# Kernel tuning notes

Hardware: AMD Instinct MI355X
Metric: run time of the kernel (lower is better)

Reference implementation:

```python
import jax, jax.numpy as jnp
import numpy as np

N_NODES = 100000
N_EDGES = 640000
D_IN = 128
D_H = 128


def setup_inputs() -> dict:
    key = jax.random.key(0)
    ks = jax.random.split(key, 24)
    def W(k, shp):
        return jax.random.normal(k, shp, dtype=jnp.float32) * 0.05
    inp = {
        "x": jax.random.normal(ks[0], (N_NODES, D_IN), dtype=jnp.float32),
        "src": jax.random.randint(ks[1], (N_EDGES,), 0, N_NODES, dtype=jnp.int32),
        "dst": jax.random.randint(ks[2], (N_EDGES,), 0, N_NODES, dtype=jnp.int32),
        "neg_src": jax.random.randint(ks[3], (N_EDGES,), 0, N_NODES, dtype=jnp.int32),
        "neg_dst": jax.random.randint(ks[4], (N_EDGES,), 0, N_NODES, dtype=jnp.int32),
        # SAGEConv layer 1/2/3: fc_self weight, fc_neigh weight (stored [in,out]), bias
        "Ws1": W(ks[5], (D_IN, D_H)), "Wn1": W(ks[6], (D_IN, D_H)), "b1": jnp.zeros((D_H,), jnp.float32),
        "Ws2": W(ks[7], (D_H, D_H)), "Wn2": W(ks[8], (D_H, D_H)), "b2": jnp.zeros((D_H,), jnp.float32),
        "Ws3": W(ks[9], (D_H, D_H)), "Wn3": W(ks[10], (D_H, D_H)), "b3": jnp.zeros((D_H,), jnp.float32),
        # MLPPredictor: W1 [2h,h], W2 [h,1]
        "Wp1": W(ks[11], (2 * D_H, D_H)), "bp1": jnp.zeros((D_H,), jnp.float32),
        "Wp2": W(ks[12], (D_H, 1)), "bp2": jnp.zeros((1,), jnp.float32),
    }
    return inp


def _sage_mean(x, src, dst, Ws, Wn, b):
    # DGL SAGEConv 'mean': rst = fc_self(h) + fc_neigh(mean_{in-neighbors}(h)) + bias
    n = x.shape[0]
    msum = jax.ops.segment_sum(x[src], dst, num_segments=n)        # [N, d]
    deg = jax.ops.segment_sum(jnp.ones_like(src, dtype=x.dtype), dst, num_segments=n)
    mean = msum / jnp.clip(deg, 1.0)[:, None]                      # zero for isolated nodes
    return x @ Ws + mean @ Wn + b


def _edge_score(h, s, d, Wp1, bp1, Wp2, bp2):
    z = jnp.concatenate([h[s], h[d]], axis=1)                      # [E, 2h]
    return (jax.nn.relu(z @ Wp1 + bp1) @ Wp2 + bp2)[:, 0]          # [E]


def reference(x, src, dst, neg_src, neg_dst,
              Ws1, Wn1, b1, Ws2, Wn2, b2, Ws3, Wn3, b3,
              Wp1, bp1, Wp2, bp2):
    h = _sage_mean(x, src, dst, Ws1, Wn1, b1)
    h = _sage_mean(h, src, dst, Ws2, Wn2, b2)
    h = _sage_mean(h, src, dst, Ws3, Wn3, b3)
    pos = _edge_score(h, src, dst, Wp1, bp1, Wp2, bp2)
    neg = _edge_score(h, neg_src, neg_dst, Wp1, bp1, Wp2, bp2)
    return (pos, neg)
```

## Files before the change

kernel.cpp:

```cpp
#include <hip/hip_runtime.h>

#define N_NODES 100000
#define N_EDGES 640000
#define D 128
#define SCAN_TILE 1024
#define SCAN_BLOCKS ((N_NODES + SCAN_TILE - 1) / SCAN_TILE)

typedef __attribute__((ext_vector_type(8))) short bf16x8;
typedef __attribute__((ext_vector_type(4))) float f32x4;

__device__ __forceinline__ unsigned short f32_to_bf16(float f) {
  union { float f; unsigned int u; } v; v.f = f;
  unsigned int u = v.u;
  unsigned int r = (u + 0x7fffu + ((u >> 16) & 1u)) >> 16;
  return (unsigned short)r;
}
__device__ __forceinline__ float bf16_lo(unsigned int u) { return __uint_as_float(u << 16); }
__device__ __forceinline__ float bf16_hi(unsigned int u) { return __uint_as_float(u & 0xffff0000u); }

__device__ __forceinline__ void acc8(float* a, uint4 r) {
  a[0] += bf16_lo(r.x); a[1] += bf16_hi(r.x);
  a[2] += bf16_lo(r.y); a[3] += bf16_hi(r.y);
  a[4] += bf16_lo(r.z); a[5] += bf16_hi(r.z);
  a[6] += bf16_lo(r.w); a[7] += bf16_hi(r.w);
}

__global__ void zero_i32(int* __restrict__ p, int n) {
  int i = blockIdx.x * blockDim.x + threadIdx.x;
  if (i < n) p[i] = 0;
}

__global__ void f32_to_bf16_vec(const float* __restrict__ in, unsigned short* __restrict__ out, int n4) {
  int i = blockIdx.x * blockDim.x + threadIdx.x;
  if (i < n4) {
    float4 v = ((const float4*)in)[i];
    ushort4 o;
    o.x = f32_to_bf16(v.x); o.y = f32_to_bf16(v.y);
    o.z = f32_to_bf16(v.z); o.w = f32_to_bf16(v.w);
    ((ushort4*)out)[i] = o;
  }
}

__global__ void transpose_w(const float* __restrict__ W0, const float* __restrict__ W1,
                            const float* __restrict__ W2, const float* __restrict__ W3,
                            const float* __restrict__ W4, const float* __restrict__ W5,
                            const float* __restrict__ W6, const float* __restrict__ W7,
                            unsigned short* __restrict__ wt) {
  int id = blockIdx.x * 256 + threadIdx.x;
  int mat = id >> 14;
  int rem = id & 16383;
  int n = rem >> 7, k = rem & 127;
  const float* Wm = mat < 4 ? (mat < 2 ? (mat == 0 ? W0 : W1) : (mat == 2 ? W2 : W3))
                            : (mat < 6 ? (mat == 4 ? W4 : W5) : (mat == 6 ? W6 : W7));
  wt[id] = f32_to_bf16(Wm[k * D + n]);
}

__global__ void hist_kernel(const int* __restrict__ dst, int* __restrict__ deg, int E) {
  int i = blockIdx.x * blockDim.x + threadIdx.x;
  if (i < E) atomicAdd(&deg[dst[i]], 1);
}

__global__ void scan_blocksum(const int* __restrict__ deg, int* __restrict__ partial, int n) {
  __shared__ int lds[256];
  const int tid = threadIdx.x;
  const int base = blockIdx.x * SCAN_TILE + tid * 4;
  int s = 0;
#pragma unroll
  for (int j = 0; j < 4; ++j) {
    int i = base + j;
    if (i < n) s += deg[i];
  }
  lds[tid] = s;
  __syncthreads();
  for (int off = 128; off > 0; off >>= 1) {
    if (tid < off) lds[tid] += lds[tid + off];
    __syncthreads();
  }
  if (tid == 0) partial[blockIdx.x] = lds[0];
}

__global__ void scan_offsets(int* __restrict__ partial, int* __restrict__ row_start, int nb, int n) {
  __shared__ int lds[128];
  const int tid = threadIdx.x;
  int v = (tid < nb) ? partial[tid] : 0;
  lds[tid] = v;
  __syncthreads();
  for (int off = 1; off < 128; off <<= 1) {
    int t = (tid >= off) ? lds[tid - off] : 0;
    __syncthreads();
    lds[tid] += t;
    __syncthreads();
  }
  if (tid < nb) partial[tid] = (tid == 0) ? 0 : lds[tid - 1];
  if (tid == 0) row_start[n] = lds[nb - 1];
}

__global__ void scan_final(const int* __restrict__ deg, const int* __restrict__ partial,
                           int* __restrict__ row_start, int n) {
  __shared__ int lds[256];
  const int tid = threadIdx.x;
  const int base = blockIdx.x * SCAN_TILE + tid * 4;
  int d[4];
  int s = 0;
#pragma unroll
  for (int j = 0; j < 4; ++j) {
    int i = base + j;
    d[j] = (i < n) ? deg[i] : 0;
    s += d[j];
  }
  lds[tid] = s;
  __syncthreads();
  for (int off = 1; off < 256; off <<= 1) {
    int t = (tid >= off) ? lds[tid - off] : 0;
    __syncthreads();
    lds[tid] += t;
    __syncthreads();
  }
  int pre = partial[blockIdx.x] + lds[tid] - s;
#pragma unroll
  for (int j = 0; j < 4; ++j) {
    int i = base + j;
    if (i < n) {
      row_start[i] = pre;
      pre += d[j];
    }
  }
}

__global__ void fill_kernel(const int* __restrict__ src, const int* __restrict__ dst,
                            const int* __restrict__ row_start, int* __restrict__ cursor,
                            int* __restrict__ esrc, int E) {
  int i = blockIdx.x * blockDim.x + threadIdx.x;
  if (i < E) {
    int d = dst[i];
    int pos = atomicAdd(&cursor[d], 1);
    esrc[row_start[d] + pos] = src[i];
  }
}

__global__ __launch_bounds__(256) void gather_mean(
    const unsigned short* __restrict__ hin,
    const int* __restrict__ row_start, const int* __restrict__ esrc,
    unsigned short* __restrict__ mean, int M) {
  const int t = blockIdx.x * blockDim.x + threadIdx.x;
  const int node = t >> 4;
  const int fl = t & 15;
  if (node >= M) return;
  const int s0 = row_start[node], s1 = row_start[node + 1];
  float ac[8] = {0.f, 0.f, 0.f, 0.f, 0.f, 0.f, 0.f, 0.f};
  for (int e = s0; e < s1; e += 8) {
    int idx[8];
#pragma unroll
    for (int j = 0; j < 8; ++j) idx[j] = esrc[min(e + j, s1 - 1)];
    uint4 r[8];
#pragma unroll
    for (int j = 0; j < 8; ++j)
      r[j] = *(const uint4*)(hin + (((size_t)idx[j]) << 7) + fl * 8);
#pragma unroll
    for (int j = 0; j < 8; ++j)
      if (e + j < s1) acc8(ac, r[j]);
  }
  const float inv = 1.0f / (float)max(s1 - s0, 1);
#pragma unroll
  for (int k = 0; k < 8; ++k) ac[k] *= inv;
  uint4 o;
  o.x = (unsigned)f32_to_bf16(ac[0]) | ((unsigned)f32_to_bf16(ac[1]) << 16);
  o.y = (unsigned)f32_to_bf16(ac[2]) | ((unsigned)f32_to_bf16(ac[3]) << 16);
  o.z = (unsigned)f32_to_bf16(ac[4]) | ((unsigned)f32_to_bf16(ac[5]) << 16);
  o.w = (unsigned)f32_to_bf16(ac[6]) | ((unsigned)f32_to_bf16(ac[7]) << 16);
  *reinterpret_cast<uint4*>(mean + (((size_t)node) << 7) + fl * 8) = o;
}

template <bool PRED>
__global__ __launch_bounds__(256) void layer_mlp(
    const unsigned short* __restrict__ hin,
    const unsigned short* __restrict__ mean,
    const unsigned short* __restrict__ Wts, const unsigned short* __restrict__ Wtn,
    const float* __restrict__ bias,
    const unsigned short* __restrict__ WtA, const unsigned short* __restrict__ WtB,
    const float* __restrict__ biasA,
    unsigned short* __restrict__ out0, unsigned short* __restrict__ out1, int M) {
  __shared__ unsigned short wl[64][136];
  __shared__ unsigned short mt[PRED ? 64 : 1][136];
  const int tid = threadIdx.x;
  const int lane = tid & 63;
  const int wave = tid >> 6;
  const int m0 = blockIdx.x * 64;
  const int row = lane & 15;
  const int q = lane >> 4;
  const int mw = m0 + wave * 16;
  const int mload = min(mw + row, M - 1);
  const int lrow = wave * 16 + row;

  unsigned short (*et)[136];
  if constexpr (PRED) et = mt; else et = wl;

  auto stage64 = [&](const unsigned short* W, int half) {
#pragma unroll
    for (int i = 0; i < 4; ++i) {
      int seg = i * 256 + tid;
      int r = seg >> 4, o = (seg & 15) * 8;
      *reinterpret_cast<bf16x8*>(&wl[r][o]) =
          *reinterpret_cast<const bf16x8*>(W + (size_t)(half * 64 + r) * D + o);
    }
  };
  auto mfma_half = [&](bf16x8* a, f32x4* accp) {
#pragma unroll
    for (int s = 0; s < 4; ++s)
#pragma unroll
      for (int t = 0; t < 4; ++t) {
        bf16x8 b = *reinterpret_cast<const bf16x8*>(&wl[t * 16 + row][s * 32 + q * 8]);
        accp[t] = __builtin_amdgcn_mfma_f32_16x16x32_bf16(a[s], b, accp[t], 0, 0, 0);
      }
  };
  auto epilogue = [&](f32x4* accp, const float* bvec, unsigned short* dst, bool prebar) {
    if (prebar) __syncthreads();
#pragma unroll
    for (int t = 0; t < 8; ++t) {
      const int col = t * 16 + row;
      const float bv = bvec ? bvec[col] : 0.f;
#pragma unroll
      for (int r = 0; r < 4; ++r)
        et[wave * 16 + q * 4 + r][col] = f32_to_bf16(accp[t][r] + bv);
    }
    __syncthreads();
#pragma unroll
    for (int i = 0; i < 4; ++i) {
      int idx = i * 256 + tid;
      int r2 = idx >> 4;
      int c8 = (idx & 15) * 8;
      int m = m0 + r2;
      if (m < M)
        *reinterpret_cast<uint4*>(dst + (size_t)m * D + c8) =
            *reinterpret_cast<const uint4*>(&et[r2][c8]);
    }
  };

  stage64(Wts, 0);
  bf16x8 ah[4], am[4];
#pragma unroll
  for (int s = 0; s < 4; ++s) {
    ah[s] = *reinterpret_cast<const bf16x8*>(hin + (size_t)mload * D + s * 32 + q * 8);
    am[s] = *reinterpret_cast<const bf16x8*>(mean + (size_t)mload * D + s * 32 + q * 8);
  }
  __syncthreads();

  f32x4 acc[8];
#pragma unroll
  for (int t = 0; t < 8; ++t) acc[t] = (f32x4){0.f, 0.f, 0.f, 0.f};

  mfma_half(ah, acc);
  __syncthreads(); stage64(Wts, 1); __syncthreads();
  mfma_half(ah, acc + 4);
  __syncthreads(); stage64(Wtn, 0); __syncthreads();
  mfma_half(am, acc);
  __syncthreads(); stage64(Wtn, 1); __syncthreads();
  mfma_half(am, acc + 4);

  if (!PRED) {
    epilogue(acc, bias, out0, true);
    return;
  }

  __syncthreads();
#pragma unroll
  for (int t = 0; t < 8; ++t) {
    const int col = t * 16 + row;
    const float bv = bias[col];
#pragma unroll
    for (int r = 0; r < 4; ++r)
      mt[wave * 16 + q * 4 + r][col] = f32_to_bf16(acc[t][r] + bv);
  }
  stage64(WtA, 0);
  __syncthreads();
  bf16x8 ap[4];
#pragma unroll
  for (int s = 0; s < 4; ++s)
    ap[s] = *reinterpret_cast<const bf16x8*>(&mt[lrow][s * 32 + q * 8]);

#pragma unroll
  for (int t = 0; t < 8; ++t) acc[t] = (f32x4){0.f, 0.f, 0.f, 0.f};
  mfma_half(ap, acc);
  __syncthreads(); stage64(WtA, 1); __syncthreads();
  mfma_half(ap, acc + 4);
  epilogue(acc, biasA, out0, false);
  __syncthreads(); stage64(WtB, 0); __syncthreads();
#pragma unroll
  for (int t = 0; t < 8; ++t) acc[t] = (f32x4){0.f, 0.f, 0.f, 0.f};
  mfma_half(ap, acc);
  __syncthreads(); stage64(WtB, 1); __syncthreads();
  mfma_half(ap, acc + 4);
  epilogue(acc, nullptr, out1, false);
}

__device__ __forceinline__ float relu_dot8(uint4 a, uint4 b, float4 w0, float4 w1) {
  return fmaxf(bf16_lo(a.x) + bf16_lo(b.x), 0.f) * w0.x +
         fmaxf(bf16_hi(a.x) + bf16_hi(b.x), 0.f) * w0.y +
         fmaxf(bf16_lo(a.y) + bf16_lo(b.y), 0.f) * w0.z +
         fmaxf(bf16_hi(a.y) + bf16_hi(b.y), 0.f) * w0.w +
         fmaxf(bf16_lo(a.z) + bf16_lo(b.z), 0.f) * w1.x +
         fmaxf(bf16_hi(a.z) + bf16_hi(b.z), 0.f) * w1.y +
         fmaxf(bf16_lo(a.w) + bf16_lo(b.w), 0.f) * w1.z +
         fmaxf(bf16_hi(a.w) + bf16_hi(b.w), 0.f) * w1.w;
}

__global__ __launch_bounds__(256) void edge_score4(
    const unsigned short* __restrict__ A, const unsigned short* __restrict__ B,
    const int* __restrict__ ps, const int* __restrict__ pd,
    const int* __restrict__ ns, const int* __restrict__ nd,
    const float* __restrict__ Wp2, const float* __restrict__ bp2,
    float* __restrict__ out, int E) {
  const int t = blockIdx.x * blockDim.x + threadIdx.x;
  const int g2 = t >> 4;
  const int fl = t & 15;
  const int g = g2 >> 1;
  const int e0 = g * 4;
  if (e0 >= E) return;
  const bool neg = (g2 & 1) != 0;
  const int* ss = neg ? ns : ps;
  const int* dd = neg ? nd : pd;
  float* op = neg ? out + E : out;

  const int4 s4 = *(const int4*)(ss + e0);
  const int4 d4 = *(const int4*)(dd + e0);
  const float4 w0 = *(const float4*)(Wp2 + fl * 8);
  const float4 w1 = *(const float4*)(Wp2 + fl * 8 + 4);
  const size_t fo = (size_t)(fl * 8);

  uint4 a0 = *(const uint4*)(A + (((size_t)s4.x << 7) + fo));
  uint4 b0 = *(const uint4*)(B + (((size_t)d4.x << 7) + fo));
  uint4 a1 = *(const uint4*)(A + (((size_t)s4.y << 7) + fo));
  uint4 b1 = *(const uint4*)(B + (((size_t)d4.y << 7) + fo));
  uint4 a2 = *(const uint4*)(A + (((size_t)s4.z << 7) + fo));
  uint4 b2 = *(const uint4*)(B + (((size_t)d4.z << 7) + fo));
  uint4 a3 = *(const uint4*)(A + (((size_t)s4.w << 7) + fo));
  uint4 b3 = *(const uint4*)(B + (((size_t)d4.w << 7) + fo));

  float p0 = relu_dot8(a0, b0, w0, w1);
  float p1 = relu_dot8(a1, b1, w0, w1);
  float p2 = relu_dot8(a2, b2, w0, w1);
  float p3 = relu_dot8(a3, b3, w0, w1);

  p0 += __shfl_xor(p0, 1); p1 += __shfl_xor(p1, 1); p2 += __shfl_xor(p2, 1); p3 += __shfl_xor(p3, 1);
  p0 += __shfl_xor(p0, 2); p1 += __shfl_xor(p1, 2); p2 += __shfl_xor(p2, 2); p3 += __shfl_xor(p3, 2);
  p0 += __shfl_xor(p0, 4); p1 += __shfl_xor(p1, 4); p2 += __shfl_xor(p2, 4); p3 += __shfl_xor(p3, 4);
  p0 += __shfl_xor(p0, 8); p1 += __shfl_xor(p1, 8); p2 += __shfl_xor(p2, 8); p3 += __shfl_xor(p3, 8);

  if (fl == 0) {
    const float bv = bp2[0];
    *reinterpret_cast<float4*>(op + e0) = make_float4(p0 + bv, p1 + bv, p2 + bv, p3 + bv);
  }
}

extern "C" void kernel_launch(void* const* d_in, const int* in_sizes, int n_in,
                              void* d_out, int out_size, void* d_ws, size_t ws_size,
                              hipStream_t stream) {
  const float* x = (const float*)d_in[0];
  const int* src = (const int*)d_in[1];
  const int* dst = (const int*)d_in[2];
  const int* nsrc = (const int*)d_in[3];
  const int* ndst = (const int*)d_in[4];
  const float* Ws1 = (const float*)d_in[5];
  const float* Wn1 = (const float*)d_in[6];
  const float* b1 = (const float*)d_in[7];
  const float* Ws2 = (const float*)d_in[8];
  const float* Wn2 = (const float*)d_in[9];
  const float* b2 = (const float*)d_in[10];
  const float* Ws3 = (const float*)d_in[11];
  const float* Wn3 = (const float*)d_in[12];
  const float* b3 = (const float*)d_in[13];
  const float* Wp1 = (const float*)d_in[14];
  const float* bp1 = (const float*)d_in[15];
  const float* Wp2 = (const float*)d_in[16];
  const float* bp2 = (const float*)d_in[17];
  float* out = (float*)d_out;

  char* ws = (char*)d_ws;
  size_t off = 0;
  auto alloc = [&](size_t bytes) -> void* {
    void* p = ws + off;
    off += (bytes + 255) & ~(size_t)255;
    return p;
  };
  const size_t NODE_F32 = sizeof(float) * (size_t)N_NODES * D;
  char* region0 = (char*)alloc(NODE_F32);
  char* region1 = (char*)alloc(NODE_F32);
  unsigned short* meanb = (unsigned short*)alloc(sizeof(unsigned short) * (size_t)N_NODES * D);
  int* row_start = (int*)alloc(sizeof(int) * (N_NODES + 1));
  int* deg = (int*)alloc(sizeof(int) * N_NODES * 2);
  int* cursor = deg + N_NODES;
  int* esrc = (int*)alloc(sizeof(int) * N_EDGES);
  int* partial = (int*)alloc(sizeof(int) * 128);
  unsigned short* wt = (unsigned short*)alloc(sizeof(unsigned short) * 8 * D * D);
  (void)ws_size;

  unsigned short* xb = (unsigned short*)region0;
  unsigned short* hA = (unsigned short*)region1;
  unsigned short* hB = hA + (size_t)N_NODES * D;
  unsigned short* Ab = xb;
  unsigned short* Bb = xb + (size_t)N_NODES * D;

  f32_to_bf16_vec<<<(N_NODES * D / 4 + 255) / 256, 256, 0, stream>>>(x, xb, N_NODES * D / 4);
  transpose_w<<<512, 256, 0, stream>>>(Ws1, Wn1, Ws2, Wn2, Ws3, Wn3, Wp1, Wp1 + D * D, wt);

  zero_i32<<<(2 * N_NODES + 255) / 256, 256, 0, stream>>>(deg, 2 * N_NODES);
  hist_kernel<<<(N_EDGES + 255) / 256, 256, 0, stream>>>(dst, deg, N_EDGES);
  scan_blocksum<<<SCAN_BLOCKS, 256, 0, stream>>>(deg, partial, N_NODES);
  scan_offsets<<<1, 128, 0, stream>>>(partial, row_start, SCAN_BLOCKS, N_NODES);
  scan_final<<<SCAN_BLOCKS, 256, 0, stream>>>(deg, partial, row_start, N_NODES);
  fill_kernel<<<(N_EDGES + 255) / 256, 256, 0, stream>>>(src, dst, row_start, cursor, esrc, N_EDGES);

  const int gatherBlocks = (N_NODES * 16 + 255) / 256;
  const int mlpBlocks = (N_NODES + 63) / 64;
  const int edgeBlocks = (2 * (N_EDGES / 4) * 16) / 256;

  gather_mean<<<gatherBlocks, 256, 0, stream>>>(xb, row_start, esrc, meanb, N_NODES);
  layer_mlp<false><<<mlpBlocks, 256, 0, stream>>>(
      xb, meanb, wt, wt + 16384, b1, nullptr, nullptr, nullptr, hA, nullptr, N_NODES);
  gather_mean<<<gatherBlocks, 256, 0, stream>>>(hA, row_start, esrc, meanb, N_NODES);
  layer_mlp<false><<<mlpBlocks, 256, 0, stream>>>(
      hA, meanb, wt + 2 * 16384, wt + 3 * 16384, b2, nullptr, nullptr, nullptr, hB, nullptr, N_NODES);
  gather_mean<<<gatherBlocks, 256, 0, stream>>>(hB, row_start, esrc, meanb, N_NODES);
  layer_mlp<true><<<mlpBlocks, 256, 0, stream>>>(
      hB, meanb, wt + 4 * 16384, wt + 5 * 16384, b3, wt + 6 * 16384, wt + 7 * 16384, bp1,
      Ab, Bb, N_NODES);
  edge_score4<<<edgeBlocks, 256, 0, stream>>>(Ab, Bb, src, dst, nsrc, ndst, Wp2, bp2, out, N_EDGES);
}
```

Before: 450.6 us.

## Score edges via destination-sorted CSR to reuse destination row

Builds a combined CSR over the positive and negative edge sets, grouped by destination and recording original edge ids. The edge scoring kernel now runs one 16-lane group per destination node, loads the B row once and gathers only the A rows of its in-neighbours, then scatters scores back by edge id. This halves the random row gathers in scoring, but adds a second histogram, scan and fill pass, extra index arrays, scattered output writes and load imbalance from varying degrees.

```diff
diff --git a/kernel.cpp b/kernel.cpp
--- a/kernel.cpp
+++ b/kernel.cpp
@@ -4,7 +4,6 @@
 #define N_EDGES 640000
 #define D 128
 #define SCAN_TILE 1024
-#define SCAN_BLOCKS ((N_NODES + SCAN_TILE - 1) / SCAN_TILE)
 
 typedef __attribute__((ext_vector_type(8))) short bf16x8;
 typedef __attribute__((ext_vector_type(4))) float f32x4;
@@ -55,9 +54,13 @@
   wt[id] = f32_to_bf16(Wm[k * D + n]);
 }
 
-__global__ void hist_kernel(const int* __restrict__ dst, int* __restrict__ deg, int E) {
+__global__ void hist2_kernel(const int* __restrict__ dst, const int* __restrict__ ndst,
+                             int* __restrict__ deg2, int E) {
   int i = blockIdx.x * blockDim.x + threadIdx.x;
-  if (i < E) atomicAdd(&deg[dst[i]], 1);
+  if (i < E) {
+    atomicAdd(&deg2[dst[i]], 1);
+    atomicAdd(&deg2[N_NODES + ndst[i]], 1);
+  }
 }
 
 __global__ void scan_blocksum(const int* __restrict__ deg, int* __restrict__ partial, int n) {
@@ -79,13 +82,13 @@
   if (tid == 0) partial[blockIdx.x] = lds[0];
 }
 
-__global__ void scan_offsets(int* __restrict__ partial, int* __restrict__ row_start, int nb, int n) {
-  __shared__ int lds[128];
+__global__ void scan_offsets256(int* __restrict__ partial, int* __restrict__ row_start, int nb, int n) {
+  __shared__ int lds[256];
   const int tid = threadIdx.x;
   int v = (tid < nb) ? partial[tid] : 0;
   lds[tid] = v;
   __syncthreads();
-  for (int off = 1; off < 128; off <<= 1) {
+  for (int off = 1; off < 256; off <<= 1) {
     int t = (tid >= off) ? lds[tid - off] : 0;
     __syncthreads();
     lds[tid] += t;
@@ -127,14 +130,22 @@
   }
 }
 
-__global__ void fill_kernel(const int* __restrict__ src, const int* __restrict__ dst,
-                            const int* __restrict__ row_start, int* __restrict__ cursor,
-                            int* __restrict__ esrc, int E) {
+__global__ void fill2_kernel(const int* __restrict__ src, const int* __restrict__ dst,
+                             const int* __restrict__ nsrc, const int* __restrict__ ndst,
+                             const int* __restrict__ rs2, int* __restrict__ cur2,
+                             int* __restrict__ esrc2, int* __restrict__ eeid2, int E) {
   int i = blockIdx.x * blockDim.x + threadIdx.x;
   if (i < E) {
     int d = dst[i];
-    int pos = atomicAdd(&cursor[d], 1);
-    esrc[row_start[d] + pos] = src[i];
+    int p = atomicAdd(&cur2[d], 1);
+    int slot = rs2[d] + p;
+    esrc2[slot] = src[i];
+    eeid2[slot] = i;
+    int nd = N_NODES + ndst[i];
+    int p2 = atomicAdd(&cur2[nd], 1);
+    int slot2 = rs2[nd] + p2;
+    esrc2[slot2] = nsrc[i];
+    eeid2[slot2] = i;
   }
 }
 
@@ -304,51 +315,72 @@
          fmaxf(bf16_hi(a.w) + bf16_hi(b.w), 0.f) * w1.w;
 }
 
-__global__ __launch_bounds__(256) void edge_score4(
+__global__ __launch_bounds__(256) void edge_score_csr(
     const unsigned short* __restrict__ A, const unsigned short* __restrict__ B,
-    const int* __restrict__ ps, const int* __restrict__ pd,
-    const int* __restrict__ ns, const int* __restrict__ nd,
+    const int* __restrict__ rs2, const int* __restrict__ esrc2, const int* __restrict__ eeid2,
     const float* __restrict__ Wp2, const float* __restrict__ bp2,
     float* __restrict__ out, int E) {
   const int t = blockIdx.x * blockDim.x + threadIdx.x;
-  const int g2 = t >> 4;
+  const int g = t >> 4;
   const int fl = t & 15;
-  const int g = g2 >> 1;
-  const int e0 = g * 4;
-  if (e0 >= E) return;
-  const bool neg = (g2 & 1) != 0;
-  const int* ss = neg ? ns : ps;
-  const int* dd = neg ? nd : pd;
-  float* op = neg ? out + E : out;
-
-  const int4 s4 = *(const int4*)(ss + e0);
-  const int4 d4 = *(const int4*)(dd + e0);
+  if (g >= 2 * N_NODES) return;
+  const int s0 = rs2[g], s1 = rs2[g + 1];
+  if (s0 >= s1) return;
+  const int node = (g < N_NODES) ? g : g - N_NODES;
+  float* op = (g < N_NODES) ? out : out + E;
+  const size_t fo = (size_t)(fl * 8);
+  const uint4 bR = *(const uint4*)(B + (((size_t)node) << 7) + fo);
   const float4 w0 = *(const float4*)(Wp2 + fl * 8);
   const float4 w1 = *(const float4*)(Wp2 + fl * 8 + 4);
-  const size_t fo = (size_t)(fl * 8);
-
-  uint4 a0 = *(const uint4*)(A + (((size_t)s4.x << 7) + fo));
-  uint4 b0 = *(const uint4*)(B + (((size_t)d4.x << 7) + fo));
-  uint4 a1 = *(const uint4*)(A + (((size_t)s4.y << 7) + fo));
-  uint4 b1 = *(const uint4*)(B + (((size_t)d4.y << 7) + fo));
-  uint4 a2 = *(const uint4*)(A + (((size_t)s4.z << 7) + fo));
-  uint4 b2 = *(const uint4*)(B + (((size_t)d4.z << 7) + fo));
-  uint4 a3 = *(const uint4*)(A + (((size_t)s4.w << 7) + fo));
-  uint4 b3 = *(const uint4*)(B + (((size_t)d4.w << 7) + fo));
-
-  float p0 = relu_dot8(a0, b0, w0, w1);
-  float p1 = relu_dot8(a1, b1, w0, w1);
-  float p2 = relu_dot8(a2, b2, w0, w1);
-  float p3 = relu_dot8(a3, b3, w0, w1);
-
-  p0 += __shfl_xor(p0, 1); p1 += __shfl_xor(p1, 1); p2 += __shfl_xor(p2, 1); p3 += __shfl_xor(p3, 1);
-  p0 += __shfl_xor(p0, 2); p1 += __shfl_xor(p1, 2); p2 += __shfl_xor(p2, 2); p3 += __shfl_xor(p3, 2);
-  p0 += __shfl_xor(p0, 4); p1 += __shfl_xor(p1, 4); p2 += __shfl_xor(p2, 4); p3 += __shfl_xor(p3, 4);
-  p0 += __shfl_xor(p0, 8); p1 += __shfl_xor(p1, 8); p2 += __shfl_xor(p2, 8); p3 += __shfl_xor(p3, 8);
-
-  if (fl == 0) {
-    const float bv = bp2[0];
-    *reinterpret_cast<float4*>(op + e0) = make_float4(p0 + bv, p1 + bv, p2 + bv, p3 + bv);
+  const float bv = bp2[0];
+
+  for (int e = s0; e < s1; e += 8) {
+    const int m = s1 - 1;
+    int i0 = esrc2[min(e + 0, m)], i1 = esrc2[min(e + 1, m)];
+    int i2 = esrc2[min(e + 2, m)], i3 = esrc2[min(e + 3, m)];
+    int i4 = esrc2[min(e + 4, m)], i5 = esrc2[min(e + 5, m)];
+    int i6 = esrc2[min(e + 6, m)], i7 = esrc2[min(e + 7, m)];
+    int d0 = eeid2[min(e + 0, m)], d1 = eeid2[min(e + 1, m)];
+    int d2 = eeid2[min(e + 2, m)], d3 = eeid2[min(e + 3, m)];
+    int d4 = eeid2[min(e + 4, m)], d5 = eeid2[min(e + 5, m)];
+    int d6 = eeid2[min(e + 6, m)], d7 = eeid2[min(e + 7, m)];
+    uint4 r0 = *(const uint4*)(A + (((size_t)i0) << 7) + fo);
+    uint4 r1 = *(const uint4*)(A + (((size_t)i1) << 7) + fo);
+    uint4 r2 = *(const uint4*)(A + (((size_t)i2) << 7) + fo);
+    uint4 r3 = *(const uint4*)(A + (((size_t)i3) << 7) + fo);
+    uint4 r4 = *(const uint4*)(A + (((size_t)i4) << 7) + fo);
+    uint4 r5 = *(const uint4*)(A + (((size_t)i5) << 7) + fo);
+    uint4 r6 = *(const uint4*)(A + (((size_t)i6) << 7) + fo);
+    uint4 r7 = *(const uint4*)(A + (((size_t)i7) << 7) + fo);
+
+    float p0 = relu_dot8(r0, bR, w0, w1);
+    float p1 = relu_dot8(r1, bR, w0, w1);
+    float p2 = relu_dot8(r2, bR, w0, w1);
+    float p3 = relu_dot8(r3, bR, w0, w1);
+    float p4 = relu_dot8(r4, bR, w0, w1);
+    float p5 = relu_dot8(r5, bR, w0, w1);
+    float p6 = relu_dot8(r6, bR, w0, w1);
+    float p7 = relu_dot8(r7, bR, w0, w1);
+
+    p0 += __shfl_xor(p0, 1); p1 += __shfl_xor(p1, 1); p2 += __shfl_xor(p2, 1); p3 += __shfl_xor(p3, 1);
+    p4 += __shfl_xor(p4, 1); p5 += __shfl_xor(p5, 1); p6 += __shfl_xor(p6, 1); p7 += __shfl_xor(p7, 1);
+    p0 += __shfl_xor(p0, 2); p1 += __shfl_xor(p1, 2); p2 += __shfl_xor(p2, 2); p3 += __shfl_xor(p3, 2);
+    p4 += __shfl_xor(p4, 2); p5 += __shfl_xor(p5, 2); p6 += __shfl_xor(p6, 2); p7 += __shfl_xor(p7, 2);
+    p0 += __shfl_xor(p0, 4); p1 += __shfl_xor(p1, 4); p2 += __shfl_xor(p2, 4); p3 += __shfl_xor(p3, 4);
+    p4 += __shfl_xor(p4, 4); p5 += __shfl_xor(p5, 4); p6 += __shfl_xor(p6, 4); p7 += __shfl_xor(p7, 4);
+    p0 += __shfl_xor(p0, 8); p1 += __shfl_xor(p1, 8); p2 += __shfl_xor(p2, 8); p3 += __shfl_xor(p3, 8);
+    p4 += __shfl_xor(p4, 8); p5 += __shfl_xor(p5, 8); p6 += __shfl_xor(p6, 8); p7 += __shfl_xor(p7, 8);
+
+    if (fl == 0) {
+      op[d0] = p0 + bv;
+      if (e + 1 < s1) op[d1] = p1 + bv;
+      if (e + 2 < s1) op[d2] = p2 + bv;
+      if (e + 3 < s1) op[d3] = p3 + bv;
+      if (e + 4 < s1) op[d4] = p4 + bv;
+      if (e + 5 < s1) op[d5] = p5 + bv;
+      if (e + 6 < s1) op[d6] = p6 + bv;
+      if (e + 7 < s1) op[d7] = p7 + bv;
+    }
   }
 }
 
@@ -386,11 +418,12 @@
   char* region0 = (char*)alloc(NODE_F32);
   char* region1 = (char*)alloc(NODE_F32);
   unsigned short* meanb = (unsigned short*)alloc(sizeof(unsigned short) * (size_t)N_NODES * D);
-  int* row_start = (int*)alloc(sizeof(int) * (N_NODES + 1));
-  int* deg = (int*)alloc(sizeof(int) * N_NODES * 2);
-  int* cursor = deg + N_NODES;
-  int* esrc = (int*)alloc(sizeof(int) * N_EDGES);
-  int* partial = (int*)alloc(sizeof(int) * 128);
+  int* rs2 = (int*)alloc(sizeof(int) * (2 * N_NODES + 1));
+  int* deg2 = (int*)alloc(sizeof(int) * 4 * N_NODES);
+  int* cur2 = deg2 + 2 * N_NODES;
+  int* esrc2 = (int*)alloc(sizeof(int) * 2 * N_EDGES);
+  int* eeid2 = (int*)alloc(sizeof(int) * 2 * N_EDGES);
+  int* partial = (int*)alloc(sizeof(int) * 256);
   unsigned short* wt = (unsigned short*)alloc(sizeof(unsigned short) * 8 * D * D);
   (void)ws_size;
 
@@ -403,26 +436,30 @@
   f32_to_bf16_vec<<<(N_NODES * D / 4 + 255) / 256, 256, 0, stream>>>(x, xb, N_NODES * D / 4);
   transpose_w<<<512, 256, 0, stream>>>(Ws1, Wn1, Ws2, Wn2, Ws3, Wn3, Wp1, Wp1 + D * D, wt);
 
-  zero_i32<<<(2 * N_NODES + 255) / 256, 256, 0, stream>>>(deg, 2 * N_NODES);
-  hist_kernel<<<(N_EDGES + 255) / 256, 256, 0, stream>>>(dst, deg, N_EDGES);
-  scan_blocksum<<<SCAN_BLOCKS, 256, 0, stream>>>(deg, partial, N_NODES);
-  scan_offsets<<<1, 128, 0, stream>>>(partial, row_start, SCAN_BLOCKS, N_NODES);
-  scan_final<<<SCAN_BLOCKS, 256, 0, stream>>>(deg, partial, row_start, N_NODES);
-  fill_kernel<<<(N_EDGES + 255) / 256, 256, 0, stream>>>(src, dst, row_start, cursor, esrc, N_EDGES);
+  const int NV = 2 * N_NODES;
+  const int SB2 = (NV + SCAN_TILE - 1) / SCAN_TILE;
+  zero_i32<<<(4 * N_NODES + 255) / 256, 256, 0, stream>>>(deg2, 4 * N_NODES);
+  hist2_kernel<<<(N_EDGES + 255) / 256, 256, 0, stream>>>(dst, ndst, deg2, N_EDGES);
+  scan_blocksum<<<SB2, 256, 0, stream>>>(deg2, partial, NV);
+  scan_offsets256<<<1, 256, 0, stream>>>(partial, rs2, SB2, NV);
+  scan_final<<<SB2, 256, 0, stream>>>(deg2, partial, rs2, NV);
+  fill2_kernel<<<(N_EDGES + 255) / 256, 256, 0, stream>>>(
+      src, dst, nsrc, ndst, rs2, cur2, esrc2, eeid2, N_EDGES);
 
   const int gatherBlocks = (N_NODES * 16 + 255) / 256;
   const int mlpBlocks = (N_NODES + 63) / 64;
-  const int edgeBlocks = (2 * (N_EDGES / 4) * 16) / 256;
-
-  gather_mean<<<gatherBlocks, 256, 0, stream>>>(xb, row_start, esrc, meanb, N_NODES);
+  const int edgeBlocks = (NV * 16 + 255) / 256;
+
+  gather_mean<<<gatherBlocks, 256, 0, stream>>>(xb, rs2, esrc2, meanb, N_NODES);
   layer_mlp<false><<<mlpBlocks, 256, 0, stream>>>(
       xb, meanb, wt, wt + 16384, b1, nullptr, nullptr, nullptr, hA, nullptr, N_NODES);
-  gather_mean<<<gatherBlocks, 256, 0, stream>>>(hA, row_start, esrc, meanb, N_NODES);
+  gather_mean<<<gatherBlocks, 256, 0, stream>>>(hA, rs2, esrc2, meanb, N_NODES);
   layer_mlp<false><<<mlpBlocks, 256, 0, stream>>>(
       hA, meanb, wt + 2 * 16384, wt + 3 * 16384, b2, nullptr, nullptr, nullptr, hB, nullptr, N_NODES);
-  gather_mean<<<gatherBlocks, 256, 0, stream>>>(hB, row_start, esrc, meanb, N_NODES);
+  gather_mean<<<gatherBlocks, 256, 0, stream>>>(hB, rs2, esrc2, meanb, N_NODES);
   layer_mlp<true><<<mlpBlocks, 256, 0, stream>>>(
       hB, meanb, wt + 4 * 16384, wt + 5 * 16384, b3, wt + 6 * 16384, wt + 7 * 16384, bp1,
       Ab, Bb, N_NODES);
-  edge_score4<<<edgeBlocks, 256, 0, stream>>>(Ab, Bb, src, dst, nsrc, ndst, Wp2, bp2, out, N_EDGES);
-}
+  edge_score_csr<<<edgeBlocks, 256, 0, stream>>>(
+      Ab, Bb, rs2, esrc2, eeid2, Wp2, bp2, out, N_EDGES);
+}
```

New measurement: 510.1 us. 1.13x slower.
